# Kernel optimization log

Measured on AMD Instinct MI355X. Metric: run time of the kernel, lower is better.

Reference implementation:

```python
import jax, jax.numpy as jnp
import numpy as np

NUM_CLASSES = 10
HIDDEN = 64
_LABEL2MASK_THRESHOL = 500


def setup_inputs() -> dict:
    key = jax.random.key(0)
    ks = jax.random.split(key, 5)
    B, h, w = 4, 60, 80
    feature1 = jax.random.normal(ks[0], (B, 512, h, w), jnp.float32)
    feature2 = jax.random.normal(ks[1], (B, 512, h // 2, w // 2), jnp.float32)
    # kaiming_normal (fan_in, relu): std = sqrt(2 / fan_in)
    w1 = jax.random.normal(ks[2], (HIDDEN, 512), jnp.float32) * np.sqrt(2.0 / 512)
    w2 = jax.random.normal(ks[3], (HIDDEN, 512), jnp.float32) * np.sqrt(2.0 / 512)
    wc = jax.random.normal(ks[4], (NUM_CLASSES + 1, HIDDEN), jnp.float32) * np.sqrt(2.0 / HIDDEN)
    b1 = jnp.zeros((HIDDEN,), jnp.float32)
    b2 = jnp.zeros((HIDDEN,), jnp.float32)
    bc = jnp.zeros((NUM_CLASSES + 1,), jnp.float32)
    return {"feature1": feature1, "feature2": feature2, "w1": w1, "b1": b1,
            "w2": w2, "b2": b2, "wc": wc, "bc": bc}


def _conv1x1(x, w, b):
    # x: (B,C,H,W), w: (O,C), b: (O,)
    return jnp.einsum('bchw,oc->bohw', x, w) + b[None, :, None, None]


def _resize2x(x, s):
    B, C, H, W = x.shape
    # torch nn.Upsample(mode='bilinear', align_corners=False) == half-pixel bilinear
    return jax.image.resize(x, (B, C, H * s, W * s), method='bilinear')


def _label2bbx(seg, num_classes, thresh):
    # seg: (B,H,W) int. Fixed-shape, fully vectorized version of the nested
    # python-loop bbox extraction. Rows with pixel count < thresh are -1.
    B, H, W = seg.shape
    cls = jnp.arange(1, num_classes, dtype=seg.dtype)        # skip background cls 0
    mask = seg[:, None, :, :] == cls[None, :, None, None]    # (B,K,H,W)
    cnt = mask.sum(axis=(2, 3))
    xs = jnp.arange(W, dtype=jnp.int32)[None, None, None, :]
    ys = jnp.arange(H, dtype=jnp.int32)[None, None, :, None]
    x1 = jnp.min(jnp.where(mask, xs, W), axis=(2, 3))
    x2 = jnp.max(jnp.where(mask, xs, -1), axis=(2, 3))
    y1 = jnp.min(jnp.where(mask, ys, H), axis=(2, 3))
    y2 = jnp.max(jnp.where(mask, ys, -1), axis=(2, 3))
    K = num_classes - 1
    bid = jnp.broadcast_to(jnp.arange(B, dtype=jnp.int32)[:, None], (B, K))
    cid = jnp.broadcast_to(cls.astype(jnp.int32)[None, :], (B, K))
    rows = jnp.stack([bid, x1.astype(jnp.int32), y1.astype(jnp.int32),
                      x2.astype(jnp.int32), y2.astype(jnp.int32), cid], axis=-1)  # (B,K,6)
    valid = (cnt >= thresh)[..., None]
    rows = jnp.where(valid, rows, -1)
    return rows.reshape(B * K, 6)


def reference(feature1, feature2, w1, b1, w2, b2, wc, bc):
    f1 = jax.nn.relu(_conv1x1(feature1, w1, b1))
    f2 = jax.nn.relu(_conv1x1(feature2, w2, b2))
    f2 = _resize2x(f2, 2)
    feat = _resize2x(f1 + f2, 8)              # (B,64,480,640)
    logits = _conv1x1(feat, wc, bc)           # (B,11,480,640)
    probability = jax.nn.softmax(logits, axis=1)
    segmentation = jnp.argmax(probability, axis=1)
    bbx = _label2bbx(segmentation, NUM_CLASSES, _LABEL2MASK_THRESHOL)
    return probability, segmentation, bbx
```

## Files before the change

### kernel.cpp

```cpp
#include <hip/hip_runtime.h>

#define BN 4
#define CIN 512
#define H1 60
#define W1 80
#define P1 4800
#define H2 30
#define W2 40
#define P2 1200
#define HID 64
#define NCLS 11
#define HF 480
#define WF 640
#define PF 307200
#define THRESH 500

#define WT1_OFF 0
#define WT2_OFF 32768
#define F2_OFF  65536
#define PART_OFF F2_OFF
#define L_OFF   (65536 + 307200)
#define PP_OFF  603136

__device__ __forceinline__ void dma16(const float* g, float* l) {
    __builtin_amdgcn_global_load_lds(
        (const __attribute__((address_space(1))) void*)g,
        (__attribute__((address_space(3))) void*)l, 16, 0, 0);
}

__global__ void k0_init(const float* __restrict__ w1, const float* __restrict__ w2,
                        float* __restrict__ ws) {
    int idx = blockIdx.x * 256 + threadIdx.x;
    if (idx < 32768) {
        int c = idx >> 6, o = idx & 63;
        ws[WT1_OFF + idx] = w1[o * CIN + c];
    } else {
        int j = idx - 32768;
        int c = j >> 6, o = j & 63;
        ws[WT2_OFF + j] = w2[o * CIN + c];
    }
}

__global__ __launch_bounds__(256, 4) void k1_conv2(const float* __restrict__ x,
                                                   const float* __restrict__ b2,
                                                   float* __restrict__ ws) {
    __shared__ float lds[8320];
    const float* wt = ws + WT2_OFF;
    float* f2o = ws + F2_OFF;
    int blk = blockIdx.x;
    int b = blk / 150, tile = blk % 150;
    int t = threadIdx.x;
    int l = t & 63, w = t >> 6;
    int q = t & 1, og = (t >> 1) & 7, ch = t >> 4;
    int o0 = og * 8;
    int p0 = tile * 8;
    const float* xb = x + (size_t)b * CIN * P2 + p0;

    auto stage = [&](int s) {
        int buf = s & 1;
#pragma unroll
        for (int j = 0; j < 2; ++j) {
            int r0 = j * 128 + w * 32;
            int r  = r0 + (l >> 1);
            int cg = (r >> 4) * 32 + s * 16 + (r & 15);
            dma16(xb + (size_t)cg * P2 + (l & 1) * 4,
                  lds + buf * 2048 + r0 * 8);
        }
    };

    float acc[4][8];
#pragma unroll
    for (int j = 0; j < 4; ++j)
#pragma unroll
        for (int i = 0; i < 8; ++i) acc[j][i] = 0.f;

    stage(0);
    __syncthreads();
    const float* wp = wt + (ch * 32) * HID + o0;
    for (int s = 0; s < 2; ++s) {
        if (s < 1) stage(s + 1);
        const float* xs = lds + (s & 1) * 2048 + ch * 128 + q * 4;
#pragma unroll 4
        for (int cc = 0; cc < 16; ++cc) {
            float4 xv = *(const float4*)(xs + cc * 8);
            const float* wr = wp + (s * 16 + cc) * HID;
            float4 wa = *(const float4*)(wr);
            float4 wb = *(const float4*)(wr + 4);
            float w8[8] = {wa.x, wa.y, wa.z, wa.w, wb.x, wb.y, wb.z, wb.w};
            float x4[4] = {xv.x, xv.y, xv.z, xv.w};
#pragma unroll
            for (int j = 0; j < 4; ++j)
#pragma unroll
                for (int i = 0; i < 8; ++i) acc[j][i] = fmaf(w8[i], x4[j], acc[j][i]);
        }
        __syncthreads();
    }
#pragma unroll
    for (int j = 0; j < 4; ++j)
#pragma unroll
        for (int i = 0; i < 8; ++i)
            lds[ch * 520 + (q * 4 + j) * 65 + o0 + i] = acc[j][i];
    __syncthreads();

    if (t < 64) {
        int px = t >> 3, oo = (t & 7) * 8;
        float v[8];
#pragma unroll
        for (int i = 0; i < 8; ++i) {
            float s = 0.f;
#pragma unroll
            for (int c = 0; c < 16; ++c) s += lds[c * 520 + px * 65 + oo + i];
            v[i] = fmaxf(s + b2[oo + i], 0.f);
        }
        float* outp = f2o + ((size_t)b * P2 + p0 + px) * HID + oo;
        *(float4*)outp = make_float4(v[0], v[1], v[2], v[3]);
        *(float4*)(outp + 4) = make_float4(v[4], v[5], v[6], v[7]);
    }
}

__global__ __launch_bounds__(256, 4) void k2a_conv1(const float* __restrict__ x,
                                                    float* __restrict__ ws) {
    __shared__ float lds[8320];
    const float* wt = ws + WT1_OFF;
    float* pp = ws + PP_OFF;
    int blk = blockIdx.x;
    int b = blk / 300;
    int rem = blk - b * 300;
    int hb = rem / 150;
    int tile = rem - hb * 150;
    int t = threadIdx.x;
    int q = t & 7, og = (t >> 3) & 7, ch = t >> 6;
    int o0 = og * 8;
    int p0 = tile * 32;
    const float* xc = x + (size_t)b * CIN * P1 + (size_t)(hb * 256 + ch * 64) * P1
                    + p0 + q * 4;
    const float* wp = wt + (size_t)(hb * 256 + ch * 64) * HID + o0;

    float acc[4][8];
#pragma unroll
    for (int j = 0; j < 4; ++j)
#pragma unroll
        for (int i = 0; i < 8; ++i) acc[j][i] = 0.f;

#pragma unroll 4
    for (int cc = 0; cc < 64; ++cc) {
        float4 xv = *(const float4*)(xc + (size_t)cc * P1);
        const float* wr = wp + cc * HID;
        float4 wa = *(const float4*)(wr);
        float4 wb = *(const float4*)(wr + 4);
        float w8[8] = {wa.x, wa.y, wa.z, wa.w, wb.x, wb.y, wb.z, wb.w};
        float x4[4] = {xv.x, xv.y, xv.z, xv.w};
#pragma unroll
        for (int j = 0; j < 4; ++j)
#pragma unroll
            for (int i = 0; i < 8; ++i) acc[j][i] = fmaf(w8[i], x4[j], acc[j][i]);
    }

#pragma unroll
    for (int j = 0; j < 4; ++j)
#pragma unroll
        for (int i = 0; i < 8; ++i)
            lds[ch * 2080 + (q * 4 + j) * 65 + o0 + i] = acc[j][i];
    __syncthreads();

    {
        int px = t >> 3;
        int oo = (t & 7) * 8;
        float v[8];
#pragma unroll
        for (int i = 0; i < 8; ++i) {
            int a = px * 65 + oo + i;
            v[i] = lds[a] + lds[2080 + a] + lds[2 * 2080 + a] + lds[3 * 2080 + a];
        }
        float* outp = pp + ((size_t)(b * 2 + hb) * P1 + p0 + px) * HID + oo;
        *(float4*)outp = make_float4(v[0], v[1], v[2], v[3]);
        *(float4*)(outp + 4) = make_float4(v[4], v[5], v[6], v[7]);
    }
}

__global__ __launch_bounds__(256) void k2b_reduce(const float* __restrict__ b1,
                                                  const float* __restrict__ wc,
                                                  const float* __restrict__ bc,
                                                  float* __restrict__ ws) {
    __shared__ float g[2080];
    const float* pp = ws + PP_OFF;
    const float* f2 = ws + F2_OFF;
    float* lout = ws + L_OFF;
    int blk = blockIdx.x;
    int b = blk / 150, tile = blk % 150;
    int t = threadIdx.x;
    int p0 = tile * 32;

    {
        int px = t >> 3;
        int oo = (t & 7) * 8;
        int p = p0 + px;
        const float* h0 = pp + ((size_t)(b * 2 + 0) * P1 + p) * HID + oo;
        const float* h1 = pp + ((size_t)(b * 2 + 1) * P1 + p) * HID + oo;
        float4 a0 = *(const float4*)h0;
        float4 a1 = *(const float4*)(h0 + 4);
        float4 c0 = *(const float4*)h1;
        float4 c1 = *(const float4*)(h1 + 4);
        float hs[8] = {a0.x + c0.x, a0.y + c0.y, a0.z + c0.z, a0.w + c0.w,
                       a1.x + c1.x, a1.y + c1.y, a1.z + c1.z, a1.w + c1.w};

        int y = p / W1, xq = p - y * W1;
        float sy = fmaf((float)y, 0.5f, -0.25f);
        float fy = floorf(sy);
        float ty = sy - fy;
        int y0 = max(0, min(H2 - 1, (int)fy));
        int y1 = max(0, min(H2 - 1, (int)fy + 1));
        float sx = fmaf((float)xq, 0.5f, -0.25f);
        float fx = floorf(sx);
        float tx = sx - fx;
        int x0 = max(0, min(W2 - 1, (int)fx));
        int x1 = max(0, min(W2 - 1, (int)fx + 1));
        float wy0 = 1.f - ty, wx0 = 1.f - tx;
        const float* f2b = f2 + (size_t)b * P2 * HID;
        const float* r00 = f2b + (y0 * W2 + x0) * HID + oo;
        const float* r01 = f2b + (y0 * W2 + x1) * HID + oo;
        const float* r10 = f2b + (y1 * W2 + x0) * HID + oo;
        const float* r11 = f2b + (y1 * W2 + x1) * HID + oo;
#pragma unroll
        for (int i = 0; i < 8; ++i) {
            float f1v = fmaxf(hs[i] + b1[oo + i], 0.f);
            float v0 = r00[i] * wx0 + r01[i] * tx;
            float v1 = r10[i] * wx0 + r11[i] * tx;
            g[px * 65 + oo + i] = f1v + (v0 * wy0 + v1 * ty);
        }
    }
    __syncthreads();

    {
        int px2 = t & 31;
        int kg = t >> 5;
        int k2i = (kg < 3) ? kg + 8 : 8;
        float l1 = bc[kg];
        float l2 = bc[k2i];
#pragma unroll 8
        for (int o = 0; o < HID; ++o) {
            float gv = g[px2 * 65 + o];
            l1 = fmaf(wc[kg * HID + o], gv, l1);
            l2 = fmaf(wc[k2i * HID + o], gv, l2);
        }
        float* lrow = lout + ((size_t)b * P1 + p0 + px2) * 12;
        lrow[kg] = l1;
        if (kg < 3) lrow[kg + 8] = l2;
        else if (kg == 3) lrow[11] = 0.f;
    }
}

__global__ __launch_bounds__(256) void k4_main(float* __restrict__ out,
                                               float* __restrict__ ws) {
    __shared__ int s_cnt[9], s_x0[9], s_y0[9], s_x1[9], s_y1[9];
    const float* l = ws + L_OFF;
    int* partb = (int*)(ws + PART_OFF);
    int t = threadIdx.x;
    if (t < 9) { s_cnt[t] = 0; s_x0[t] = WF; s_y0[t] = HF; s_x1[t] = -1; s_y1[t] = -1; }
    __syncthreads();

    int fl = blockIdx.x * 256 + t;
    int b = fl / PF;
    int r = fl - b * PF;
    int Y = r / WF;
    int X = r - Y * WF;

    float sy = fmaf((float)Y, 0.125f, -0.4375f);
    float fy = floorf(sy);
    float ty = sy - fy;
    int y0 = max(0, min(H1 - 1, (int)fy));
    int y1 = max(0, min(H1 - 1, (int)fy + 1));
    float sx = fmaf((float)X, 0.125f, -0.4375f);
    float fx = floorf(sx);
    float tx = sx - fx;
    int x0 = max(0, min(W1 - 1, (int)fx));
    int x1 = max(0, min(W1 - 1, (int)fx + 1));
    float wy0 = 1.f - ty, wx0 = 1.f - tx;

    const float* lb = l + (size_t)b * P1 * 12;
    const float4* q00 = (const float4*)(lb + (y0 * W1 + x0) * 12);
    const float4* q01 = (const float4*)(lb + (y0 * W1 + x1) * 12);
    const float4* q10 = (const float4*)(lb + (y1 * W1 + x0) * 12);
    const float4* q11 = (const float4*)(lb + (y1 * W1 + x1) * 12);
    float l00[12], l01[12], l10[12], l11[12];
#pragma unroll
    for (int j = 0; j < 3; ++j) {
        ((float4*)l00)[j] = q00[j];
        ((float4*)l01)[j] = q01[j];
        ((float4*)l10)[j] = q10[j];
        ((float4*)l11)[j] = q11[j];
    }
    float li[11];
#pragma unroll
    for (int k = 0; k < 11; ++k) {
        float v0 = l00[k] * wx0 + l01[k] * tx;
        float v1 = l10[k] * wx0 + l11[k] * tx;
        li[k] = v0 * wy0 + v1 * ty;
    }
    int am = 0;
    float bm = li[0];
#pragma unroll
    for (int k = 1; k < 11; ++k) {
        if (li[k] > bm) { bm = li[k]; am = k; }
    }
    float e[11];
    float s = 0.f;
#pragma unroll
    for (int k = 0; k < 11; ++k) { e[k] = __expf(li[k] - bm); s += e[k]; }
    float rs = 1.f / s;
    size_t ob = (size_t)b * NCLS * PF + r;
#pragma unroll
    for (int k = 0; k < 11; ++k) out[ob + (size_t)k * PF] = e[k] * rs;
    out[(size_t)BN * NCLS * PF + fl] = (float)am;

    int lane = t & 63;
    int X0 = X & ~63;
    for (int c = 1; c <= 9; ++c) {
        unsigned long long m = __ballot(am == c);
        if (m != 0ULL && lane == 0) {
            int ci = c - 1;
            atomicAdd(&s_cnt[ci], (int)__popcll(m));
            atomicMin(&s_x0[ci], X0 + __builtin_ctzll(m));
            atomicMax(&s_x1[ci], X0 + 63 - __builtin_clzll(m));
            atomicMin(&s_y0[ci], Y);
            atomicMax(&s_y1[ci], Y);
        }
    }
    __syncthreads();
    if (t < 9) {
        int* pr = partb + blockIdx.x * 45 + t * 5;
        pr[0] = s_cnt[t];
        pr[1] = s_x0[t];
        pr[2] = s_y0[t];
        pr[3] = s_x1[t];
        pr[4] = s_y1[t];
    }
}

__global__ void k5_bbx(float* __restrict__ out, const float* __restrict__ ws) {
    const int* partb = (const int*)(ws + PART_OFF);
    int b = blockIdx.x / 9, c = blockIdx.x % 9;
    int t = threadIdx.x;
    int cnt = 0, mnx = WF, mny = HF, mxx = -1, mxy = -1;
    for (int i = t; i < 1200; i += 64) {
        const int* pr = partb + (size_t)(b * 1200 + i) * 45 + c * 5;
        cnt += pr[0];
        mnx = min(mnx, pr[1]);
        mny = min(mny, pr[2]);
        mxx = max(mxx, pr[3]);
        mxy = max(mxy, pr[4]);
    }
    for (int sft = 32; sft; sft >>= 1) {
        cnt += __shfl_xor(cnt, sft);
        mnx = min(mnx, __shfl_xor(mnx, sft));
        mny = min(mny, __shfl_xor(mny, sft));
        mxx = max(mxx, __shfl_xor(mxx, sft));
        mxy = max(mxy, __shfl_xor(mxy, sft));
    }
    if (t == 0) {
        float* row = out + (size_t)BN * NCLS * PF + (size_t)BN * PF + (size_t)(b * 9 + c) * 6;
        bool ok = cnt >= THRESH;
        row[0] = ok ? (float)b : -1.f;
        row[1] = ok ? (float)mnx : -1.f;
        row[2] = ok ? (float)mny : -1.f;
        row[3] = ok ? (float)mxx : -1.f;
        row[4] = ok ? (float)mxy : -1.f;
        row[5] = ok ? (float)(c + 1) : -1.f;
    }
}

extern "C" void kernel_launch(void* const* d_in, const int* in_sizes, int n_in,
                              void* d_out, int out_size, void* d_ws, size_t ws_size,
                              hipStream_t stream) {
    const float* f1 = (const float*)d_in[0];
    const float* f2 = (const float*)d_in[1];
    const float* w1 = (const float*)d_in[2];
    const float* b1 = (const float*)d_in[3];
    const float* w2 = (const float*)d_in[4];
    const float* b2 = (const float*)d_in[5];
    const float* wc = (const float*)d_in[6];
    const float* bc = (const float*)d_in[7];
    float* out = (float*)d_out;
    float* ws = (float*)d_ws;

    k0_init<<<dim3(256), dim3(256), 0, stream>>>(w1, w2, ws);
    k1_conv2<<<dim3(600), dim3(256), 0, stream>>>(f2, b2, ws);
    k2a_conv1<<<dim3(1200), dim3(256), 0, stream>>>(f1, ws);
    k2b_reduce<<<dim3(600), dim3(256), 0, stream>>>(b1, wc, bc, ws);
    k4_main<<<dim3(4800), dim3(256), 0, stream>>>(out, ws);
    k5_bbx<<<dim3(36), dim3(64), 0, stream>>>(out, ws);
}
```

Measured before the change: 180.4 us.

## Fuse conv1 channel-split and reduce kernels with register double-buffered loads

Merges the conv1 partial-sum kernel and the reduce/upsample/classifier kernel into one, so each block accumulates all 512 input channels (4 groups of 128) and does the bias, ReLU, f2 bilinear add and class logits in-block. This removes the partial-sum round trip through global memory and one launch. The channel loop now software-pipelines loads of 8 channels into registers ahead of compute. The grid halves to 600 blocks with longer per-thread loops, so there is less parallelism to hide latency, and register pressure rises from the two 8-entry float4 buffers.

```diff
diff --git a/kernel.cpp b/kernel.cpp
--- a/kernel.cpp
+++ b/kernel.cpp
@@ -20,7 +20,6 @@
 #define F2_OFF  65536
 #define PART_OFF F2_OFF
 #define L_OFF   (65536 + 307200)
-#define PP_OFF  603136
 
 __device__ __forceinline__ void dma16(const float* g, float* l) {
     __builtin_amdgcn_global_load_lds(
@@ -118,92 +117,71 @@
     }
 }
 
-__global__ __launch_bounds__(256, 4) void k2a_conv1(const float* __restrict__ x,
-                                                    float* __restrict__ ws) {
+__global__ __launch_bounds__(256, 4) void k2_conv1(const float* __restrict__ x,
+                                                   const float* __restrict__ b1,
+                                                   const float* __restrict__ wc,
+                                                   const float* __restrict__ bc,
+                                                   float* __restrict__ ws) {
     __shared__ float lds[8320];
     const float* wt = ws + WT1_OFF;
-    float* pp = ws + PP_OFF;
-    int blk = blockIdx.x;
-    int b = blk / 300;
-    int rem = blk - b * 300;
-    int hb = rem / 150;
-    int tile = rem - hb * 150;
-    int t = threadIdx.x;
-    int q = t & 7, og = (t >> 3) & 7, ch = t >> 6;
-    int o0 = og * 8;
-    int p0 = tile * 32;
-    const float* xc = x + (size_t)b * CIN * P1 + (size_t)(hb * 256 + ch * 64) * P1
-                    + p0 + q * 4;
-    const float* wp = wt + (size_t)(hb * 256 + ch * 64) * HID + o0;
-
-    float acc[4][8];
-#pragma unroll
-    for (int j = 0; j < 4; ++j)
-#pragma unroll
-        for (int i = 0; i < 8; ++i) acc[j][i] = 0.f;
-
-#pragma unroll 4
-    for (int cc = 0; cc < 64; ++cc) {
-        float4 xv = *(const float4*)(xc + (size_t)cc * P1);
-        const float* wr = wp + cc * HID;
-        float4 wa = *(const float4*)(wr);
-        float4 wb = *(const float4*)(wr + 4);
-        float w8[8] = {wa.x, wa.y, wa.z, wa.w, wb.x, wb.y, wb.z, wb.w};
-        float x4[4] = {xv.x, xv.y, xv.z, xv.w};
-#pragma unroll
-        for (int j = 0; j < 4; ++j)
-#pragma unroll
-            for (int i = 0; i < 8; ++i) acc[j][i] = fmaf(w8[i], x4[j], acc[j][i]);
-    }
-
-#pragma unroll
-    for (int j = 0; j < 4; ++j)
-#pragma unroll
-        for (int i = 0; i < 8; ++i)
-            lds[ch * 2080 + (q * 4 + j) * 65 + o0 + i] = acc[j][i];
-    __syncthreads();
-
-    {
-        int px = t >> 3;
-        int oo = (t & 7) * 8;
-        float v[8];
-#pragma unroll
-        for (int i = 0; i < 8; ++i) {
-            int a = px * 65 + oo + i;
-            v[i] = lds[a] + lds[2080 + a] + lds[2 * 2080 + a] + lds[3 * 2080 + a];
-        }
-        float* outp = pp + ((size_t)(b * 2 + hb) * P1 + p0 + px) * HID + oo;
-        *(float4*)outp = make_float4(v[0], v[1], v[2], v[3]);
-        *(float4*)(outp + 4) = make_float4(v[4], v[5], v[6], v[7]);
-    }
-}
-
-__global__ __launch_bounds__(256) void k2b_reduce(const float* __restrict__ b1,
-                                                  const float* __restrict__ wc,
-                                                  const float* __restrict__ bc,
-                                                  float* __restrict__ ws) {
-    __shared__ float g[2080];
-    const float* pp = ws + PP_OFF;
     const float* f2 = ws + F2_OFF;
     float* lout = ws + L_OFF;
     int blk = blockIdx.x;
     int b = blk / 150, tile = blk % 150;
     int t = threadIdx.x;
+    int q = t & 7, og = (t >> 3) & 7, ch = t >> 6;
+    int o0 = og * 8;
     int p0 = tile * 32;
+    const float* xc = x + (size_t)b * CIN * P1 + (size_t)(ch * 128) * P1 + p0 + q * 4;
+    const float* wp = wt + (size_t)(ch * 128) * HID + o0;
+
+    float acc[4][8];
+#pragma unroll
+    for (int j = 0; j < 4; ++j)
+#pragma unroll
+        for (int i = 0; i < 8; ++i) acc[j][i] = 0.f;
+
+    auto loadg = [&](float4* xb, int g) {
+        const float* p = xc + (size_t)g * (8 * P1);
+#pragma unroll
+        for (int i = 0; i < 8; ++i) xb[i] = *(const float4*)(p + (size_t)i * P1);
+    };
+    auto computeg = [&](const float4* xb, int g) {
+        const float* wr0 = wp + g * 8 * HID;
+#pragma unroll
+        for (int i = 0; i < 8; ++i) {
+            float4 wa = *(const float4*)(wr0 + i * HID);
+            float4 wb = *(const float4*)(wr0 + i * HID + 4);
+            float w8[8] = {wa.x, wa.y, wa.z, wa.w, wb.x, wb.y, wb.z, wb.w};
+            float x4[4] = {xb[i].x, xb[i].y, xb[i].z, xb[i].w};
+#pragma unroll
+            for (int j = 0; j < 4; ++j)
+#pragma unroll
+                for (int i2 = 0; i2 < 8; ++i2) acc[j][i2] = fmaf(w8[i2], x4[j], acc[j][i2]);
+        }
+    };
+
+    float4 xA[8], xB[8];
+    loadg(xA, 0);
+#pragma unroll 1
+    for (int g = 0; g < 16; g += 2) {
+        loadg(xB, min(g + 1, 15));
+        computeg(xA, g);
+        loadg(xA, min(g + 2, 15));
+        computeg(xB, g + 1);
+    }
+
+#pragma unroll
+    for (int j = 0; j < 4; ++j)
+#pragma unroll
+        for (int i = 0; i < 8; ++i)
+            lds[ch * 2080 + (q * 4 + j) * 65 + o0 + i] = acc[j][i];
+    __syncthreads();
 
     {
         int px = t >> 3;
         int oo = (t & 7) * 8;
         int p = p0 + px;
-        const float* h0 = pp + ((size_t)(b * 2 + 0) * P1 + p) * HID + oo;
-        const float* h1 = pp + ((size_t)(b * 2 + 1) * P1 + p) * HID + oo;
-        float4 a0 = *(const float4*)h0;
-        float4 a1 = *(const float4*)(h0 + 4);
-        float4 c0 = *(const float4*)h1;
-        float4 c1 = *(const float4*)(h1 + 4);
-        float hs[8] = {a0.x + c0.x, a0.y + c0.y, a0.z + c0.z, a0.w + c0.w,
-                       a1.x + c1.x, a1.y + c1.y, a1.z + c1.z, a1.w + c1.w};
-
         int y = p / W1, xq = p - y * W1;
         float sy = fmaf((float)y, 0.5f, -0.25f);
         float fy = floorf(sy);
@@ -223,10 +201,12 @@
         const float* r11 = f2b + (y1 * W2 + x1) * HID + oo;
 #pragma unroll
         for (int i = 0; i < 8; ++i) {
-            float f1v = fmaxf(hs[i] + b1[oo + i], 0.f);
+            int a = px * 65 + oo + i;
+            float s = lds[a] + lds[2080 + a] + lds[2 * 2080 + a] + lds[3 * 2080 + a];
+            float f1v = fmaxf(s + b1[oo + i], 0.f);
             float v0 = r00[i] * wx0 + r01[i] * tx;
             float v1 = r10[i] * wx0 + r11[i] * tx;
-            g[px * 65 + oo + i] = f1v + (v0 * wy0 + v1 * ty);
+            lds[a] = f1v + (v0 * wy0 + v1 * ty);
         }
     }
     __syncthreads();
@@ -239,7 +219,7 @@
         float l2 = bc[k2i];
 #pragma unroll 8
         for (int o = 0; o < HID; ++o) {
-            float gv = g[px2 * 65 + o];
+            float gv = lds[px2 * 65 + o];
             l1 = fmaf(wc[kg * HID + o], gv, l1);
             l2 = fmaf(wc[k2i * HID + o], gv, l2);
         }
@@ -385,8 +365,7 @@
 
     k0_init<<<dim3(256), dim3(256), 0, stream>>>(w1, w2, ws);
     k1_conv2<<<dim3(600), dim3(256), 0, stream>>>(f2, b2, ws);
-    k2a_conv1<<<dim3(1200), dim3(256), 0, stream>>>(f1, ws);
-    k2b_reduce<<<dim3(600), dim3(256), 0, stream>>>(b1, wc, bc, ws);
+    k2_conv1<<<dim3(600), dim3(256), 0, stream>>>(f1, b1, wc, bc, ws);
     k4_main<<<dim3(4800), dim3(256), 0, stream>>>(out, ws);
     k5_bbx<<<dim3(36), dim3(64), 0, stream>>>(out, ws);
 }
```

Measured after the change: 185.0 us. 2.5% more time.

## Stage conv1 weights in LDS and double-buffer feature loads in registers

Applied to the files above, without the earlier changes.

The first conv kernel now copies its weight slice into shared memory with async 16-byte copies and reads weights from LDS instead of global memory. Feature loads are split into groups of 8 channels and double-buffered in registers, so the next group's loads are in flight while the current group is computed. Shared memory grows to 64KB and launch bounds drop to 2 blocks per CU, which lowers occupancy and raises register pressure. The last iteration issues redundant reloads of group 7.

```diff
diff --git a/kernel.cpp b/kernel.cpp
--- a/kernel.cpp
+++ b/kernel.cpp
@@ -118,10 +118,10 @@
     }
 }
 
-__global__ __launch_bounds__(256, 4) void k2a_conv1(const float* __restrict__ x,
+__global__ __launch_bounds__(256, 2) void k2a_conv1(const float* __restrict__ x,
                                                     float* __restrict__ ws) {
-    __shared__ float lds[8320];
-    const float* wt = ws + WT1_OFF;
+    __shared__ float lds[16384];
+    const float* wtg = ws + WT1_OFF;
     float* pp = ws + PP_OFF;
     int blk = blockIdx.x;
     int b = blk / 300;
@@ -129,12 +129,29 @@
     int hb = rem / 150;
     int tile = rem - hb * 150;
     int t = threadIdx.x;
+    int l = t & 63;
     int q = t & 7, og = (t >> 3) & 7, ch = t >> 6;
     int o0 = og * 8;
     int p0 = tile * 32;
     const float* xc = x + (size_t)b * CIN * P1 + (size_t)(hb * 256 + ch * 64) * P1
                     + p0 + q * 4;
-    const float* wp = wt + (size_t)(hb * 256 + ch * 64) * HID + o0;
+
+    float4 xA[8], xB[8];
+    auto loadg = [&](float4* xb, int g) {
+        const float* p = xc + (size_t)g * (8 * P1);
+#pragma unroll
+        for (int i = 0; i < 8; ++i) xb[i] = *(const float4*)(p + (size_t)i * P1);
+    };
+
+    loadg(xA, 0);
+
+    {
+        const float* src = wtg + hb * 16384 + ch * 4096;
+#pragma unroll
+        for (int i = 0; i < 16; ++i)
+            dma16(src + i * 256 + l * 4, lds + ch * 4096 + i * 256);
+    }
+    __syncthreads();
 
     float acc[4][8];
 #pragma unroll
@@ -142,20 +159,31 @@
 #pragma unroll
         for (int i = 0; i < 8; ++i) acc[j][i] = 0.f;
 
-#pragma unroll 4
-    for (int cc = 0; cc < 64; ++cc) {
-        float4 xv = *(const float4*)(xc + (size_t)cc * P1);
-        const float* wr = wp + cc * HID;
-        float4 wa = *(const float4*)(wr);
-        float4 wb = *(const float4*)(wr + 4);
-        float w8[8] = {wa.x, wa.y, wa.z, wa.w, wb.x, wb.y, wb.z, wb.w};
-        float x4[4] = {xv.x, xv.y, xv.z, xv.w};
-#pragma unroll
-        for (int j = 0; j < 4; ++j)
-#pragma unroll
-            for (int i = 0; i < 8; ++i) acc[j][i] = fmaf(w8[i], x4[j], acc[j][i]);
-    }
-
+    const float* wl = lds + ch * 4096 + o0;
+    auto computeg = [&](const float4* xb, int g) {
+        const float* wr0 = wl + g * 8 * 64;
+#pragma unroll
+        for (int i = 0; i < 8; ++i) {
+            float4 wa  = *(const float4*)(wr0 + i * 64);
+            float4 wb4 = *(const float4*)(wr0 + i * 64 + 4);
+            float w8[8] = {wa.x, wa.y, wa.z, wa.w, wb4.x, wb4.y, wb4.z, wb4.w};
+            float x4[4] = {xb[i].x, xb[i].y, xb[i].z, xb[i].w};
+#pragma unroll
+            for (int j = 0; j < 4; ++j)
+#pragma unroll
+                for (int i2 = 0; i2 < 8; ++i2) acc[j][i2] = fmaf(w8[i2], x4[j], acc[j][i2]);
+        }
+    };
+
+#pragma unroll 1
+    for (int g = 0; g < 8; g += 2) {
+        loadg(xB, min(g + 1, 7));
+        computeg(xA, g);
+        loadg(xA, min(g + 2, 7));
+        computeg(xB, g + 1);
+    }
+
+    __syncthreads();
 #pragma unroll
     for (int j = 0; j < 4; ++j)
 #pragma unroll
```

New measurement: 167.3 us (median of 3 runs). 7.3% less time.
